# Performance work log

Measured on AMD Instinct MI355X. Metric: run time of the kernel, lower is better.

## Reference

```python
import jax, jax.numpy as jnp
import numpy as np

N_NODES = 100000
N_EDGES = 1600000
IN_DIM, HID_DIM, OUT_DIM = 128, 256, 128


def gcn_conv(x, edge_index, W, b):
    """PyG GCNConv: add self-loops, sym-normalize, linear transform, scatter-add, bias."""
    n = x.shape[0]
    loop = jnp.arange(n, dtype=edge_index.dtype)
    src = jnp.concatenate([edge_index[0], loop])  # message source (x_j)
    dst = jnp.concatenate([edge_index[1], loop])  # aggregation target
    deg = jax.ops.segment_sum(jnp.ones_like(dst, dtype=x.dtype), dst, num_segments=n)
    dinv = jnp.where(deg > 0, deg ** -0.5, 0.0).astype(x.dtype)
    norm = dinv[src] * dinv[dst]                  # [E+N]
    h = x @ W                                     # [N, out]
    msg = h[src] * norm[:, None]                  # [E+N, out] gather
    out = jax.ops.segment_sum(msg, dst, num_segments=n)  # scatter-add
    return out + b


def setup_inputs() -> dict:
    key = jax.random.key(0)
    k = jax.random.split(key, 6)
    x = jax.random.normal(k[0], (N_NODES, IN_DIM), dtype=jnp.float32)
    edge_index = jax.random.randint(k[1], (2, N_EDGES), 0, N_NODES, dtype=jnp.int64)
    # Glorot-ish init for weights
    W1 = jax.random.normal(k[2], (IN_DIM, HID_DIM), dtype=jnp.float32) * (1.0 / np.sqrt(IN_DIM))
    b1 = jnp.zeros((HID_DIM,), dtype=jnp.float32)
    W2 = jax.random.normal(k[3], (HID_DIM, OUT_DIM), dtype=jnp.float32) * (1.0 / np.sqrt(HID_DIM))
    b2 = jnp.zeros((OUT_DIM,), dtype=jnp.float32)
    return {"x": x, "edge_index": edge_index, "W1": W1, "b1": b1, "W2": W2, "b2": b2}


def reference(x, edge_index, W1, b1, W2, b2):
    h = gcn_conv(x, edge_index, W1, b1)
    h = jax.nn.relu(h)  # relu between layers (drop_rate=0 -> no dropout)
    h = gcn_conv(h, edge_index, W2, b2)
    return h
```

## Files before the change

### kernel.cpp

```cpp
#include <hip/hip_runtime.h>
#include <hip/hip_bf16.h>

#define N_NODES 100000
#define N_EDGES 1600000
#define IN_DIM 128
#define HID_DIM 256
#define OUT_DIM 128
#define NB ((N_NODES + 1023) / 1024)
#define DCHUNK 12500
#define EGRID 8192
#define CAP 64
#define FFGRID 782
#define NSTRIP (N_NODES / 16)
#define GWAVES 2048

#define PB_ZERO 391
#define PB_PREP 258
#define PB_CONVX 12500
#define PB_TOTAL (PB_ZERO + PB_PREP + PB_CONVX)

typedef __attribute__((ext_vector_type(8))) short bf16x8;
typedef __attribute__((ext_vector_type(4))) float f32x4;
typedef __attribute__((ext_vector_type(4))) float float4v;
typedef unsigned long long ull;
typedef unsigned short u16;

__device__ __forceinline__ float bf2f(u16 u) {
  union { unsigned int i; float f; } c; c.i = ((unsigned int)u) << 16; return c.f;
}
__device__ __forceinline__ u16 f2bf(float f) {
  __hip_bfloat16 h = __float2bfloat16(f);
  return *(u16*)&h;
}

__global__ void detect_kernel(const int* __restrict__ ei,
                              const unsigned int* __restrict__ xw,
                              int* __restrict__ flags) {
  int lane = threadIdx.x;
  const long long* p = (const long long*)ei;
  long long v = p[lane & 15];
  int ebad = (lane < 16) && (v < 0 || v >= N_NODES);
  ull ebm = __ballot(ebad);
  int isf32 = 0;
  #pragma unroll
  for (int i = 0; i < 4; ++i) {
    unsigned int ex = (xw[lane * 4 + i] >> 7) & 0xFF;
    if (ex >= 0xC0) isf32 = 1;
  }
  ull fbm = __ballot(isf32);
  if (lane == 0) {
    flags[0] = (ebm == 0) ? 1 : 0;
    flags[1] = (fbm != 0) ? 1 : 0;
  }
}

__device__ __forceinline__ int edge_at(const int* ei, int idx, int mode) {
  return mode ? (int)((const long long*)ei)[idx] : ei[idx];
}

__global__ void prologue_kernel(const void* __restrict__ x,
                                const void* __restrict__ W1, const void* __restrict__ b1,
                                const void* __restrict__ W2, const void* __restrict__ b2,
                                const int* __restrict__ flags,
                                int* __restrict__ cnt,
                                u16* __restrict__ Wt1, u16* __restrict__ Wt2,
                                u16* __restrict__ b1c, u16* __restrict__ b2c,
                                u16* __restrict__ xc) {
  int b = blockIdx.x, tid = threadIdx.x;
  if (b < PB_ZERO) {
    int i = b * 256 + tid;
    if (i < N_NODES) cnt[i] = 0;
  } else if (b < PB_ZERO + PB_PREP) {
    int i = (b - PB_ZERO) * 256 + tid;
    int f = flags[1];
    auto cvt = [&](const void* P, int idx) -> u16 {
      return f ? f2bf(((const float*)P)[idx]) : ((const u16*)P)[idx];
    };
    if (i < 32768) {
      int k = i >> 8, n = i & 255;
      Wt1[n * 128 + k] = cvt(W1, i);
    } else if (i < 65536) {
      int j = i - 32768;
      int k = j >> 7, n = j & 127;
      Wt2[n * 256 + k] = cvt(W2, j);
    } else if (i < 65792) {
      b1c[i - 65536] = cvt(b1, i - 65536);
    } else if (i < 65920) {
      b2c[i - 65792] = cvt(b2, i - 65792);
    }
  } else {
    int i = (b - PB_ZERO - PB_PREP) * 256 + tid;
    if (i >= N_NODES * IN_DIM / 4) return;
    if (flags[1]) {
      float4v v = ((const float4v*)x)[i];
      ull w = (ull)f2bf(v.x) | ((ull)f2bf(v.y) << 16) | ((ull)f2bf(v.z) << 32) |
              ((ull)f2bf(v.w) << 48);
      ((ull*)xc)[i] = w;
    } else {
      ((ull*)xc)[i] = ((const ull*)x)[i];
    }
  }
}

__global__ void fill_fixed_kernel(const int* __restrict__ ei,
                                  const int* __restrict__ flags,
                                  int* __restrict__ cnt, int* __restrict__ csrf) {
  int tg = blockIdx.x * 256 + threadIdx.x;
  int base = tg * 8;
  if (base >= N_EDGES) return;
  int dv[8], sv[8];
  if (flags[0]) {
    const longlong2* ps = (const longlong2*)ei + (base >> 1);
    const longlong2* pd = (const longlong2*)ei + ((N_EDGES + base) >> 1);
    #pragma unroll
    for (int k = 0; k < 4; ++k) {
      longlong2 s2 = ps[k], d2 = pd[k];
      sv[2 * k] = (int)s2.x; sv[2 * k + 1] = (int)s2.y;
      dv[2 * k] = (int)d2.x; dv[2 * k + 1] = (int)d2.y;
    }
  } else {
    int4 s0 = *(const int4*)(ei + base);
    int4 s1 = *(const int4*)(ei + base + 4);
    int4 d0 = *(const int4*)(ei + N_EDGES + base);
    int4 d1 = *(const int4*)(ei + N_EDGES + base + 4);
    sv[0] = s0.x; sv[1] = s0.y; sv[2] = s0.z; sv[3] = s0.w;
    sv[4] = s1.x; sv[5] = s1.y; sv[6] = s1.z; sv[7] = s1.w;
    dv[0] = d0.x; dv[1] = d0.y; dv[2] = d0.z; dv[3] = d0.w;
    dv[4] = d1.x; dv[5] = d1.y; dv[6] = d1.z; dv[7] = d1.w;
  }
  int p8[8];
  #pragma unroll
  for (int k = 0; k < 8; ++k) p8[k] = atomicAdd(&cnt[dv[k]], 1);
  #pragma unroll
  for (int k = 0; k < 8; ++k)
    if (p8[k] < CAP) csrf[dv[k] * CAP + p8[k]] = sv[k];
}

__global__ void degnorm_kernel(const int* __restrict__ cnt, float* __restrict__ dinv) {
  int i = blockIdx.x * 256 + threadIdx.x;
  if (i < N_NODES) dinv[i] = rsqrtf((float)(cnt[i] + 1));
}

__global__ void count_kernel(const int* __restrict__ ei, const int* __restrict__ flags,
                             int* __restrict__ deg) {
  int g = blockIdx.x & 7;
  unsigned lo = (unsigned)(g * DCHUNK);
  unsigned hi = lo + DCHUNK; if (hi > N_NODES) hi = N_NODES;
  int m = flags[0];
  int stride = (EGRID >> 3) * 256;
  for (int e = (blockIdx.x >> 3) * 256 + threadIdx.x; e < N_EDGES; e += stride) {
    unsigned d = (unsigned)edge_at(ei, N_EDGES + e, m);
    if (d >= lo && d < hi) atomicAdd(&deg[d], 1);
  }
}

__global__ void zero_kernel(int* p, int n) {
  int i = blockIdx.x * 256 + threadIdx.x;
  if (i < n) p[i] = 0;
}

__global__ __launch_bounds__(1024) void bsum_kernel(const int* __restrict__ deg,
                                                    int* __restrict__ bsum, int n) {
  __shared__ int ws[16];
  int tid = threadIdx.x, lane = tid & 63, wid = tid >> 6;
  int idx = blockIdx.x * 1024 + tid;
  int v = (idx < n) ? deg[idx] : 0;
  #pragma unroll
  for (int o = 32; o > 0; o >>= 1) v += __shfl_down(v, o);
  if (lane == 0) ws[wid] = v;
  __syncthreads();
  if (tid == 0) {
    int r = 0;
    #pragma unroll
    for (int i = 0; i < 16; ++i) r += ws[i];
    bsum[blockIdx.x] = r;
  }
}

__global__ void bscan_kernel(const int* __restrict__ bsum, int* __restrict__ boff,
                             int* __restrict__ total, int nb) {
  int lane = threadIdx.x;
  int carry = 0;
  for (int c = 0; c < (nb + 63) / 64; ++c) {
    int idx = c * 64 + lane;
    int v = (idx < nb) ? bsum[idx] : 0;
    int x = v;
    #pragma unroll
    for (int o = 1; o < 64; o <<= 1) {
      int y = __shfl_up(x, o);
      if (lane >= o) x += y;
    }
    if (idx < nb) boff[idx] = carry + x - v;
    carry += __shfl(x, 63);
  }
  if (lane == 0) *total = carry;
}

__global__ __launch_bounds__(1024) void bfill_kernel(const int* __restrict__ deg,
                                                     const int* __restrict__ boff,
                                                     int* __restrict__ off,
                                                     int* __restrict__ cur,
                                                     float* __restrict__ dinv, int n) {
  __shared__ int wsum[16];
  __shared__ int wpre[16];
  int tid = threadIdx.x, lane = tid & 63, wid = tid >> 6;
  int idx = blockIdx.x * 1024 + tid;
  int v = (idx < n) ? deg[idx] : 0;
  int x = v;
  #pragma unroll
  for (int o = 1; o < 64; o <<= 1) {
    int y = __shfl_up(x, o);
    if (lane >= o) x += y;
  }
  if (lane == 63) wsum[wid] = x;
  __syncthreads();
  if (tid == 0) {
    int r = 0;
    #pragma unroll
    for (int i = 0; i < 16; ++i) { wpre[i] = r; r += wsum[i]; }
  }
  __syncthreads();
  int excl = boff[blockIdx.x] + wpre[wid] + x - v;
  if (idx < n) {
    off[idx] = excl;
    cur[idx] = excl;
    dinv[idx] = rsqrtf((float)(v + 1));
  }
}

__global__ void fill_kernel(const int* __restrict__ ei, const int* __restrict__ flags,
                            int* __restrict__ cur, int* __restrict__ csr) {
  int g = blockIdx.x & 7;
  unsigned lo = (unsigned)(g * DCHUNK);
  unsigned hi = lo + DCHUNK; if (hi > N_NODES) hi = N_NODES;
  int m = flags[0];
  int stride = (EGRID >> 3) * 256;
  for (int e = (blockIdx.x >> 3) * 256 + threadIdx.x; e < N_EDGES; e += stride) {
    unsigned d = (unsigned)edge_at(ei, N_EDGES + e, m);
    if (d >= lo && d < hi) {
      int s = edge_at(ei, e, m);
      int p = atomicAdd(&cur[d], 1);
      if ((unsigned)p < N_EDGES) csr[p] = s;
    }
  }
}

template <bool BIAS, bool OUTF32, bool FIXED>
__global__ __launch_bounds__(256) void agg_kernel(
    const u16* __restrict__ V, const int* __restrict__ off,
    const int* __restrict__ csr, const float* __restrict__ dinv,
    const u16* __restrict__ bias, void* __restrict__ outv) {
  int d = (blockIdx.x * 256 + threadIdx.x) >> 6;
  int lane = threadIdx.x & 63;
  if (d >= N_NODES) return;
  int du = __builtin_amdgcn_readfirstlane(d);
  int grp = lane >> 4, sub = lane & 15;
  float dv = dinv[du];
  bf16x8 w0 = *(const bf16x8*)(V + (size_t)du * 128 + sub * 8);
  float self_s = (grp == 0) ? dv : 0.0f;
  float a[8];
  #pragma unroll
  for (int k = 0; k < 8; ++k) a[k] = self_s * bf2f((u16)w0[k]);
  int e, e1;
  if (FIXED) {
    int c = __builtin_amdgcn_readfirstlane(off[du]);
    if (c > CAP) c = CAP;
    e = du * CAP;
    e1 = e + c;
  } else {
    e  = __builtin_amdgcn_readfirstlane(off[du]);
    e1 = __builtin_amdgcn_readfirstlane(off[du + 1]);
  }
  for (; e + 8 <= e1; e += 8) {
    int sA = csr[e + grp];
    int sB = csr[e + 4 + grp];
    float dsA = dinv[sA];
    float dsB = dinv[sB];
    bf16x8 wA = *(const bf16x8*)(V + (size_t)sA * 128 + sub * 8);
    bf16x8 wB = *(const bf16x8*)(V + (size_t)sB * 128 + sub * 8);
    #pragma unroll
    for (int k = 0; k < 8; ++k) a[k] = fmaf(dsA, bf2f((u16)wA[k]), a[k]);
    #pragma unroll
    for (int k = 0; k < 8; ++k) a[k] = fmaf(dsB, bf2f((u16)wB[k]), a[k]);
  }
  for (; e + 4 <= e1; e += 4) {
    int s = csr[e + grp];
    float ds = dinv[s];
    bf16x8 w = *(const bf16x8*)(V + (size_t)s * 128 + sub * 8);
    #pragma unroll
    for (int k = 0; k < 8; ++k) a[k] = fmaf(ds, bf2f((u16)w[k]), a[k]);
  }
  int rem = e1 - e;
  if (rem > 0) {
    int ee = e + (grp < rem ? grp : 0);
    int s = csr[ee];
    float ds = (grp < rem) ? dinv[s] : 0.0f;
    bf16x8 w = *(const bf16x8*)(V + (size_t)s * 128 + sub * 8);
    #pragma unroll
    for (int k = 0; k < 8; ++k) a[k] = fmaf(ds, bf2f((u16)w[k]), a[k]);
  }
  #pragma unroll
  for (int k = 0; k < 8; ++k) {
    a[k] += __shfl_xor(a[k], 16);
    a[k] += __shfl_xor(a[k], 32);
    a[k] *= dv;
  }
  if (BIAS) {
    bf16x8 bv = *(const bf16x8*)(bias + sub * 8);
    #pragma unroll
    for (int k = 0; k < 8; ++k) a[k] += bf2f((u16)bv[k]);
  }
  if (OUTF32) {
    if (grp < 2) {
      f32x4 o4;
      #pragma unroll
      for (int r = 0; r < 4; ++r) o4[r] = a[grp * 4 + r];
      *(f32x4*)((float*)outv + (size_t)du * 128 + sub * 8 + grp * 4) = o4;
    }
  } else {
    if (grp == 0) {
      bf16x8 ob;
      #pragma unroll
      for (int k = 0; k < 8; ++k) ob[k] = (short)f2bf(a[k]);
      *(bf16x8*)((u16*)outv + (size_t)du * 128 + sub * 8) = ob;
    }
  }
}

__global__ __launch_bounds__(256) void mlp1_kernel(
    const u16* __restrict__ xa, const u16* __restrict__ Wt1,
    const u16* __restrict__ b1, u16* __restrict__ h) {
  __shared__ u16 B[32768];
  int tid = threadIdx.x;
  #pragma unroll
  for (int j = 0; j < 16; ++j) {
    int i = j * 256 + tid;
    int row = i >> 4, blk = i & 15;
    int phys = (row << 4) | (blk ^ (row & 15));
    *(bf16x8*)&B[phys * 8] = *(const bf16x8*)(Wt1 + (size_t)i * 8);
  }
  __syncthreads();
  int wid = tid >> 6, lane = tid & 63, ml = lane & 15, q = lane >> 4;
  for (int s = blockIdx.x * 4 + wid; s < NSTRIP; s += GWAVES) {
    const short* Ar = (const short*)xa + (size_t)(s * 16 + ml) * IN_DIM + q * 8;
    f32x4 acc[16] = {};
    #pragma unroll
    for (int k0 = 0; k0 < IN_DIM; k0 += 32) {
      bf16x8 a = *(const bf16x8*)(Ar + k0);
      int kb = k0 >> 3;
      #pragma unroll
      for (int t = 0; t < 16; ++t) {
        int brow = t * 16 + ml;
        const u16* Bp = &B[(((unsigned)brow << 4) | (unsigned)((kb + q) ^ ml)) * 8];
        acc[t] = __builtin_amdgcn_mfma_f32_16x16x32_bf16(a, *(const bf16x8*)Bp, acc[t], 0, 0, 0);
      }
    }
    size_t hb = (size_t)s * 16 * HID_DIM;
    #pragma unroll
    for (int t = 0; t < 16; ++t) {
      float bv = bf2f(b1[t * 16 + ml]);
      #pragma unroll
      for (int r = 0; r < 4; ++r)
        h[hb + (size_t)(q * 4 + r) * HID_DIM + t * 16 + ml] =
            f2bf(fmaxf(acc[t][r] + bv, 0.0f));
    }
  }
}

__global__ __launch_bounds__(256) void mlp2_kernel(
    const u16* __restrict__ h, const u16* __restrict__ Wt2, u16* __restrict__ xg) {
  __shared__ u16 B[32768];
  int tid = threadIdx.x;
  #pragma unroll
  for (int j = 0; j < 16; ++j) {
    int i = j * 256 + tid;
    int row = i >> 5, blk = i & 31;
    int phys = (row << 5) | (blk ^ (row & 15));
    *(bf16x8*)&B[phys * 8] = *(const bf16x8*)(Wt2 + (size_t)i * 8);
  }
  __syncthreads();
  int wid = tid >> 6, lane = tid & 63, ml = lane & 15, q = lane >> 4;
  for (int s = blockIdx.x * 4 + wid; s < NSTRIP; s += GWAVES) {
    const short* Ar = (const short*)h + (size_t)(s * 16 + ml) * HID_DIM + q * 8;
    f32x4 acc[8] = {};
    #pragma unroll
    for (int k0 = 0; k0 < HID_DIM; k0 += 32) {
      bf16x8 a = *(const bf16x8*)(Ar + k0);
      int kb = k0 >> 3;
      #pragma unroll
      for (int t = 0; t < 8; ++t) {
        int brow = t * 16 + ml;
        const u16* Bp = &B[(((unsigned)brow << 5) | (unsigned)((kb + q) ^ ml)) * 8];
        acc[t] = __builtin_amdgcn_mfma_f32_16x16x32_bf16(a, *(const bf16x8*)Bp, acc[t], 0, 0, 0);
      }
    }
    size_t gb = (size_t)s * 16 * OUT_DIM;
    #pragma unroll
    for (int t = 0; t < 8; ++t) {
      #pragma unroll
      for (int r = 0; r < 4; ++r)
        xg[gb + (size_t)(q * 4 + r) * OUT_DIM + t * 16 + ml] = f2bf(acc[t][r]);
    }
  }
}

extern "C" void kernel_launch(void* const* d_in, const int* in_sizes, int n_in,
                              void* d_out, int out_size, void* d_ws, size_t ws_size,
                              hipStream_t stream) {
  const void* x  = d_in[0];
  const int*  ei = (const int*)d_in[1];
  const void* W1 = d_in[2];
  const void* b1 = d_in[3];
  const void* W2 = d_in[4];
  const void* b2 = d_in[5];

  char* wsb = (char*)d_ws;

  {
    size_t o = 0;
    auto carve = [&](size_t bytes) {
      o = (o + 511) & ~(size_t)511;
      void* p = wsb + o;
      o += bytes;
      return p;
    };
    int*   flags = (int*)carve(8);
    int*   cnt  = (int*)carve((size_t)N_NODES * 4);
    float* dinv = (float*)carve((size_t)N_NODES * 4);
    int*   csrf = (int*)carve((size_t)N_NODES * CAP * 4);
    u16*   Wt1 = (u16*)carve((size_t)IN_DIM * HID_DIM * 2);
    u16*   Wt2 = (u16*)carve((size_t)HID_DIM * OUT_DIM * 2);
    u16*   b1c = (u16*)carve((size_t)HID_DIM * 2);
    u16*   b2c = (u16*)carve((size_t)OUT_DIM * 2);
    u16*   xc  = (u16*)carve((size_t)N_NODES * 128 * 2);
    u16*   xa  = (u16*)carve((size_t)N_NODES * 128 * 2);
    u16*   h   = (u16*)d_out;
    if (o <= ws_size) {
      detect_kernel<<<1, 64, 0, stream>>>(ei, (const unsigned int*)x, flags);
      prologue_kernel<<<PB_TOTAL, 256, 0, stream>>>(x, W1, b1, W2, b2, flags,
                                                    cnt, Wt1, Wt2, b1c, b2c, xc);
      fill_fixed_kernel<<<FFGRID, 256, 0, stream>>>(ei, flags, cnt, csrf);
      degnorm_kernel<<<(N_NODES + 255) / 256, 256, 0, stream>>>(cnt, dinv);
      agg_kernel<false, false, true>
          <<<(N_NODES * 64) / 256, 256, 0, stream>>>(xc, cnt, csrf, dinv, nullptr, xa);
      mlp1_kernel<<<512, 256, 0, stream>>>(xa, Wt1, b1c, h);
      mlp2_kernel<<<512, 256, 0, stream>>>(h, Wt2, xa);
      agg_kernel<true, true, true>
          <<<(N_NODES * 64) / 256, 256, 0, stream>>>(xa, cnt, csrf, dinv, b2c, d_out);
      return;
    }
  }

  size_t o = 0;
  auto carve = [&](size_t bytes) {
    o = (o + 511) & ~(size_t)511;
    void* p = wsb + o;
    o += bytes;
    return p;
  };
  int*   flags = (int*)carve(8);
  int*   deg  = (int*)carve((size_t)N_NODES * 4);
  int*   off  = (int*)carve((size_t)(N_NODES + 1) * 4);
  int*   cur  = (int*)carve((size_t)N_NODES * 4);
  float* dinv = (float*)carve((size_t)N_NODES * 4);
  int*   csr  = (int*)carve((size_t)N_EDGES * 4);
  int*   bsum = (int*)carve((size_t)NB * 4);
  int*   boff = (int*)carve((size_t)NB * 4);
  u16*   Wt1 = (u16*)carve((size_t)IN_DIM * HID_DIM * 2);
  u16*   Wt2 = (u16*)carve((size_t)HID_DIM * OUT_DIM * 2);
  u16*   b1c = (u16*)carve((size_t)HID_DIM * 2);
  u16*   b2c = (u16*)carve((size_t)OUT_DIM * 2);
  u16*   xc  = (u16*)carve((size_t)N_NODES * 128 * 2);
  u16*   xa  = (u16*)carve((size_t)N_NODES * 128 * 2);
  u16*   h   = (u16*)d_out;

  detect_kernel<<<1, 64, 0, stream>>>(ei, (const unsigned int*)x, flags);
  zero_kernel<<<(N_NODES + 255) / 256, 256, 0, stream>>>(deg, N_NODES);
  prologue_kernel<<<PB_TOTAL, 256, 0, stream>>>(x, W1, b1, W2, b2, flags,
                                                deg, Wt1, Wt2, b1c, b2c, xc);
  count_kernel<<<EGRID, 256, 0, stream>>>(ei, flags, deg);
  bsum_kernel<<<NB, 1024, 0, stream>>>(deg, bsum, N_NODES);
  bscan_kernel<<<1, 64, 0, stream>>>(bsum, boff, off + N_NODES, NB);
  bfill_kernel<<<NB, 1024, 0, stream>>>(deg, boff, off, cur, dinv, N_NODES);
  fill_kernel<<<EGRID, 256, 0, stream>>>(ei, flags, cur, csr);

  agg_kernel<false, false, false>
      <<<(N_NODES * 64) / 256, 256, 0, stream>>>(xc, off, csr, dinv, nullptr, xa);
  mlp1_kernel<<<512, 256, 0, stream>>>(xa, Wt1, b1c, h);
  mlp2_kernel<<<512, 256, 0, stream>>>(h, Wt2, xa);
  agg_kernel<true, true, false>
      <<<(N_NODES * 64) / 256, 256, 0, stream>>>(xa, off, csr, dinv, b2c, d_out);
}
```

Before: 414.0 us.

## Fuse detection with counter zeroing and merge CSR fill into prep kernel

Result: faster. 349.5 us (-15.6%).

```diff
diff --git a/kernel.cpp b/kernel.cpp
--- a/kernel.cpp
+++ b/kernel.cpp
@@ -10,9 +10,13 @@
 #define DCHUNK 12500
 #define EGRID 8192
 #define CAP 64
-#define FFGRID 782
 #define NSTRIP (N_NODES / 16)
 #define GWAVES 2048
+
+#define FILLB 8192
+#define FPREP 258
+#define FCONVX 12500
+#define FUSED_TOTAL (FILLB + FPREP + FCONVX)
 
 #define PB_ZERO 391
 #define PB_PREP 258
@@ -33,29 +37,112 @@
   return *(u16*)&h;
 }
 
-__global__ void detect_kernel(const int* __restrict__ ei,
-                              const unsigned int* __restrict__ xw,
-                              int* __restrict__ flags) {
-  int lane = threadIdx.x;
-  const long long* p = (const long long*)ei;
-  long long v = p[lane & 15];
-  int ebad = (lane < 16) && (v < 0 || v >= N_NODES);
-  ull ebm = __ballot(ebad);
-  int isf32 = 0;
-  #pragma unroll
-  for (int i = 0; i < 4; ++i) {
-    unsigned int ex = (xw[lane * 4 + i] >> 7) & 0xFF;
-    if (ex >= 0xC0) isf32 = 1;
-  }
-  ull fbm = __ballot(isf32);
-  if (lane == 0) {
-    flags[0] = (ebm == 0) ? 1 : 0;
-    flags[1] = (fbm != 0) ? 1 : 0;
+__global__ void detect_zero_kernel(const int* __restrict__ ei,
+                                   const unsigned int* __restrict__ xw,
+                                   int* __restrict__ flags, int* __restrict__ cnt) {
+  int tid = threadIdx.x;
+  int i = blockIdx.x * 256 + tid;
+  if (i < N_NODES) cnt[i] = 0;
+  if (blockIdx.x == 0 && tid < 64) {
+    const long long* p = (const long long*)ei;
+    long long v = p[tid & 15];
+    int ebad = (tid < 16) && (v < 0 || v >= N_NODES);
+    ull ebm = __ballot(ebad);
+    int isf32 = 0;
+    #pragma unroll
+    for (int k = 0; k < 4; ++k) {
+      unsigned int ex = (xw[tid * 4 + k] >> 7) & 0xFF;
+      if (ex >= 0xC0) isf32 = 1;
+    }
+    ull fbm = __ballot(isf32);
+    if (tid == 0) {
+      flags[0] = (ebm == 0) ? 1 : 0;
+      flags[1] = (fbm != 0) ? 1 : 0;
+    }
   }
 }
 
 __device__ __forceinline__ int edge_at(const int* ei, int idx, int mode) {
   return mode ? (int)((const long long*)ei)[idx] : ei[idx];
+}
+
+__global__ void fill_prep_kernel(const int* __restrict__ ei, const void* __restrict__ x,
+                                 const void* __restrict__ W1, const void* __restrict__ b1,
+                                 const void* __restrict__ W2, const void* __restrict__ b2,
+                                 const int* __restrict__ flags,
+                                 int* __restrict__ cnt, int* __restrict__ csrf,
+                                 u16* __restrict__ Wt1, u16* __restrict__ Wt2,
+                                 u16* __restrict__ b1c, u16* __restrict__ b2c,
+                                 u16* __restrict__ xc) {
+  int b = blockIdx.x, tid = threadIdx.x;
+  if (b < FILLB) {
+    int g = b & 7;
+    unsigned lo = (unsigned)(g * DCHUNK);
+    unsigned hi = lo + DCHUNK; if (hi > N_NODES) hi = N_NODES;
+    int stride = (FILLB >> 3) * 256;
+    int e0 = (b >> 3) * 256 + tid;
+    if (flags[0]) {
+      const long long* s64 = (const long long*)ei;
+      const long long* d64 = s64 + N_EDGES;
+      for (int e = e0; e < N_EDGES; e += stride) {
+        unsigned d = (unsigned)(int)d64[e];
+        if (d >= lo && d < hi) {
+          int s = (int)s64[e];
+          int p = atomicAdd(&cnt[d], 1);
+          if (p < CAP) csrf[d * CAP + p] = s;
+        }
+      }
+    } else {
+      const int* d32 = ei + N_EDGES;
+      for (int e = e0; e < N_EDGES; e += stride) {
+        unsigned d = (unsigned)d32[e];
+        if (d >= lo && d < hi) {
+          int s = ei[e];
+          int p = atomicAdd(&cnt[d], 1);
+          if (p < CAP) csrf[d * CAP + p] = s;
+        }
+      }
+    }
+  } else if (b < FILLB + FPREP) {
+    int i = (b - FILLB) * 256 + tid;
+    int f = flags[1];
+    auto cvt = [&](const void* P, int idx) -> u16 {
+      return f ? f2bf(((const float*)P)[idx]) : ((const u16*)P)[idx];
+    };
+    if (i < 32768) {
+      int k = i >> 8, n = i & 255;
+      Wt1[n * 128 + k] = cvt(W1, i);
+    } else if (i < 65536) {
+      int j = i - 32768;
+      int k = j >> 7, n = j & 127;
+      Wt2[n * 256 + k] = cvt(W2, j);
+    } else if (i < 65792) {
+      b1c[i - 65536] = cvt(b1, i - 65536);
+    } else if (i < 65920) {
+      b2c[i - 65792] = cvt(b2, i - 65792);
+    }
+  } else {
+    int i = (b - FILLB - FPREP) * 256 + tid;
+    if (i >= N_NODES * IN_DIM / 4) return;
+    if (flags[1]) {
+      float4v v = ((const float4v*)x)[i];
+      ull w = (ull)f2bf(v.x) | ((ull)f2bf(v.y) << 16) | ((ull)f2bf(v.z) << 32) |
+              ((ull)f2bf(v.w) << 48);
+      ((ull*)xc)[i] = w;
+    } else {
+      ((ull*)xc)[i] = ((const ull*)x)[i];
+    }
+  }
+}
+
+__global__ void degnorm_kernel(const int* __restrict__ cnt, float* __restrict__ dinv) {
+  int i = blockIdx.x * 256 + threadIdx.x;
+  if (i < N_NODES) dinv[i] = rsqrtf((float)(cnt[i] + 1));
+}
+
+__global__ void zero_kernel(int* p, int n) {
+  int i = blockIdx.x * 256 + threadIdx.x;
+  if (i < n) p[i] = 0;
 }
 
 __global__ void prologue_kernel(const void* __restrict__ x,
@@ -102,45 +189,6 @@
   }
 }
 
-__global__ void fill_fixed_kernel(const int* __restrict__ ei,
-                                  const int* __restrict__ flags,
-                                  int* __restrict__ cnt, int* __restrict__ csrf) {
-  int tg = blockIdx.x * 256 + threadIdx.x;
-  int base = tg * 8;
-  if (base >= N_EDGES) return;
-  int dv[8], sv[8];
-  if (flags[0]) {
-    const longlong2* ps = (const longlong2*)ei + (base >> 1);
-    const longlong2* pd = (const longlong2*)ei + ((N_EDGES + base) >> 1);
-    #pragma unroll
-    for (int k = 0; k < 4; ++k) {
-      longlong2 s2 = ps[k], d2 = pd[k];
-      sv[2 * k] = (int)s2.x; sv[2 * k + 1] = (int)s2.y;
-      dv[2 * k] = (int)d2.x; dv[2 * k + 1] = (int)d2.y;
-    }
-  } else {
-    int4 s0 = *(const int4*)(ei + base);
-    int4 s1 = *(const int4*)(ei + base + 4);
-    int4 d0 = *(const int4*)(ei + N_EDGES + base);
-    int4 d1 = *(const int4*)(ei + N_EDGES + base + 4);
-    sv[0] = s0.x; sv[1] = s0.y; sv[2] = s0.z; sv[3] = s0.w;
-    sv[4] = s1.x; sv[5] = s1.y; sv[6] = s1.z; sv[7] = s1.w;
-    dv[0] = d0.x; dv[1] = d0.y; dv[2] = d0.z; dv[3] = d0.w;
-    dv[4] = d1.x; dv[5] = d1.y; dv[6] = d1.z; dv[7] = d1.w;
-  }
-  int p8[8];
-  #pragma unroll
-  for (int k = 0; k < 8; ++k) p8[k] = atomicAdd(&cnt[dv[k]], 1);
-  #pragma unroll
-  for (int k = 0; k < 8; ++k)
-    if (p8[k] < CAP) csrf[dv[k] * CAP + p8[k]] = sv[k];
-}
-
-__global__ void degnorm_kernel(const int* __restrict__ cnt, float* __restrict__ dinv) {
-  int i = blockIdx.x * 256 + threadIdx.x;
-  if (i < N_NODES) dinv[i] = rsqrtf((float)(cnt[i] + 1));
-}
-
 __global__ void count_kernel(const int* __restrict__ ei, const int* __restrict__ flags,
                              int* __restrict__ deg) {
   int g = blockIdx.x & 7;
@@ -152,11 +200,6 @@
     unsigned d = (unsigned)edge_at(ei, N_EDGES + e, m);
     if (d >= lo && d < hi) atomicAdd(&deg[d], 1);
   }
-}
-
-__global__ void zero_kernel(int* p, int n) {
-  int i = blockIdx.x * 256 + threadIdx.x;
-  if (i < n) p[i] = 0;
 }
 
 __global__ __launch_bounds__(1024) void bsum_kernel(const int* __restrict__ deg,
@@ -436,10 +479,9 @@
     u16*   xa  = (u16*)carve((size_t)N_NODES * 128 * 2);
     u16*   h   = (u16*)d_out;
     if (o <= ws_size) {
-      detect_kernel<<<1, 64, 0, stream>>>(ei, (const unsigned int*)x, flags);
-      prologue_kernel<<<PB_TOTAL, 256, 0, stream>>>(x, W1, b1, W2, b2, flags,
-                                                    cnt, Wt1, Wt2, b1c, b2c, xc);
-      fill_fixed_kernel<<<FFGRID, 256, 0, stream>>>(ei, flags, cnt, csrf);
+      detect_zero_kernel<<<391, 256, 0, stream>>>(ei, (const unsigned int*)x, flags, cnt);
+      fill_prep_kernel<<<FUSED_TOTAL, 256, 0, stream>>>(ei, x, W1, b1, W2, b2, flags,
+                                                        cnt, csrf, Wt1, Wt2, b1c, b2c, xc);
       degnorm_kernel<<<(N_NODES + 255) / 256, 256, 0, stream>>>(cnt, dinv);
       agg_kernel<false, false, true>
           <<<(N_NODES * 64) / 256, 256, 0, stream>>>(xc, cnt, csrf, dinv, nullptr, xa);
@@ -474,8 +516,7 @@
   u16*   xa  = (u16*)carve((size_t)N_NODES * 128 * 2);
   u16*   h   = (u16*)d_out;
 
-  detect_kernel<<<1, 64, 0, stream>>>(ei, (const unsigned int*)x, flags);
-  zero_kernel<<<(N_NODES + 255) / 256, 256, 0, stream>>>(deg, N_NODES);
+  detect_zero_kernel<<<391, 256, 0, stream>>>(ei, (const unsigned int*)x, flags, deg);
   prologue_kernel<<<PB_TOTAL, 256, 0, stream>>>(x, W1, b1, W2, b2, flags,
                                                 deg, Wt1, Wt2, b1c, b2c, xc);
   count_kernel<<<EGRID, 256, 0, stream>>>(ei, flags, deg);
```
